# Optimization experiments

Hardware: AMD Instinct MI355X
Metric: run time of the kernel (lower is better)

Reference implementation:

```python
import jax, jax.numpy as jnp
import numpy as np

B = 2048      # number of scenes (samples)
A = 64        # max agents per scene
D = 128       # latent_size (embed dim)
H = 4         # heads (hardcoded in module)
HD = D // H   # head dim = 32
NEG = -1e9


def setup_inputs() -> dict:
    key = jax.random.key(0)
    k1, k2, k3, k4 = jax.random.split(key, 4)
    # flat ragged agent features; only the first sum(agents) rows are 'real'
    att_in = jax.random.normal(k1, (B * A, D), dtype=jnp.float32)
    agents_per_sample = jax.random.randint(k2, (B,), 1, A + 1)  # each scene has >=1 agent
    s = 1.0 / np.sqrt(D)
    w_in = jax.random.uniform(k3, (3 * D, D), minval=-s, maxval=s, dtype=jnp.float32)
    b_in = jnp.zeros((3 * D,), dtype=jnp.float32)
    w_out = jax.random.uniform(k4, (D, D), minval=-s, maxval=s, dtype=jnp.float32)
    b_out = jnp.zeros((D,), dtype=jnp.float32)
    return {"att_in": att_in, "w_in": w_in, "b_in": b_in,
            "w_out": w_out, "b_out": b_out, "agents_per_sample": agents_per_sample}


def reference(att_in, w_in, b_in, w_out, b_out, agents_per_sample):
    # scatter flat ragged rows into padded [B, A, D] (same as padded_att_in[mask] = att_in)
    offsets = jnp.cumsum(agents_per_sample) - agents_per_sample          # exclusive prefix sum
    idx = offsets[:, None] + jnp.arange(A)[None, :]                      # [B, A] flat row index
    mask = jnp.arange(A)[None, :] < agents_per_sample[:, None]          # [B, A] valid-agent mask
    padded = jnp.take(att_in, idx, axis=0) * mask[..., None].astype(att_in.dtype)
    # fused in-projection (nn.MultiheadAttention in_proj)
    qkv = padded @ w_in.T + b_in                                        # [B, A, 3D]
    q, k, v = jnp.split(qkv, 3, axis=-1)
    q = q.reshape(B, A, H, HD)
    k = k.reshape(B, A, H, HD)
    v = v.reshape(B, A, H, HD)
    scores = jnp.einsum('bqhd,bkhd->bhqk', q, k) / np.sqrt(HD).astype(q.dtype)
    # key_padding_mask: padded keys excluded from softmax
    scores = jnp.where(mask[:, None, None, :], scores, NEG)
    attn = jax.nn.softmax(scores, axis=-1)
    ctx = jnp.einsum('bhqk,bkhd->bqhd', attn, v).reshape(B, A, D)
    out = (ctx @ w_out.T + b_out) * mask[..., None].astype(ctx.dtype)   # zero out padded rows (torch slices them off)
    return out
```

## Files before the change

kernel.cpp:

```cpp
#include <hip/hip_runtime.h>
#include <hip/hip_bf16.h>

typedef __bf16 bf16;
typedef __bf16 bf16x4 __attribute__((ext_vector_type(4)));
typedef __bf16 bf16x8 __attribute__((ext_vector_type(8)));
typedef float  f32x4  __attribute__((ext_vector_type(4)));

#define NEG_INF (-1e9f)

#define N_SCENES 2048

__global__ __launch_bounds__(256) void prep_kernel(
    const float* __restrict__ w_in, const float* __restrict__ w_out,
    const int* __restrict__ agents,
    bf16* __restrict__ w_in_b, bf16* __restrict__ w_out_b, int* __restrict__ offs)
{
    __shared__ int tot[256];
    const int t = threadIdx.x;
    if (blockIdx.x == 0) {
        int loc[8]; int s = 0;
        #pragma unroll
        for (int j = 0; j < 8; ++j) { loc[j] = agents[t * 8 + j]; s += loc[j]; }
        tot[t] = s;
        __syncthreads();
        for (int o = 1; o < 256; o <<= 1) {
            int v = (t >= o) ? tot[t - o] : 0;
            __syncthreads();
            tot[t] += v;
            __syncthreads();
        }
        int run = tot[t] - s;
        #pragma unroll
        for (int j = 0; j < 8; ++j) { offs[t * 8 + j] = run; run += loc[j]; }
    } else {
        int i = (blockIdx.x - 1) * 1024 + t * 4;
        float4 v; bf16* dst;
        if (i < 49152) { v = *(const float4*)(w_in + i);            dst = w_in_b + i; }
        else           { v = *(const float4*)(w_out + (i - 49152)); dst = w_out_b + (i - 49152); }
        bf16x4 o = { (bf16)v.x, (bf16)v.y, (bf16)v.z, (bf16)v.w };
        *(bf16x4*)dst = o;
    }
}

__global__ __launch_bounds__(256, 2) void attn_kernel(
    const float* __restrict__ att_in,
    const float* __restrict__ b_in, const float* __restrict__ b_out,
    const bf16* __restrict__ w_in_b, const bf16* __restrict__ w_out_b,
    const int* __restrict__ agents, const int* __restrict__ offs,
    float* __restrict__ out)
{
    __shared__ bf16 s_x[64 * 128];
    __shared__ bf16 s_qk[64 * 256];
    __shared__ bf16 s_vT[128 * 64];
    __shared__ bf16 s_ctx[64 * 128];

    const int b    = blockIdx.x;
    const int tid  = threadIdx.x;
    const int lane = tid & 63;
    const int w    = tid >> 6;
    const int r    = lane & 15;
    const int qd   = lane >> 4;
    const int nb   = agents[b];
    const int off  = offs[b];

    for (int i = tid; i < 64 * 32; i += 256) {
        int row = i >> 5, c4 = i & 31;
        float4 v = make_float4(0.f, 0.f, 0.f, 0.f);
        if (row < nb)
            v = *(const float4*)(att_in + (((size_t)(off + row)) << 7) + (c4 << 2));
        int chunk = c4 >> 1, half = c4 & 1;
        int c = chunk ^ (row & 15);
        bf16x4 o = { (bf16)v.x, (bf16)v.y, (bf16)v.z, (bf16)v.w };
        *(bf16x4*)(s_x + row * 128 + c * 8 + half * 4) = o;
    }
    __syncthreads();

    bf16x8 xa[4][4];
    #pragma unroll
    for (int mt = 0; mt < 4; ++mt)
        #pragma unroll
        for (int ks = 0; ks < 4; ++ks) {
            int row = mt * 16 + r;
            int c = (ks * 4 + qd) ^ r;
            xa[mt][ks] = *(const bf16x8*)(s_x + row * 128 + c * 8);
        }
    #pragma unroll
    for (int t6 = 0; t6 < 6; ++t6) {
        int nt = w + t6 * 4;
        int j0 = nt * 16;
        bf16x8 wb[4];
        #pragma unroll
        for (int ks = 0; ks < 4; ++ks)
            wb[ks] = *(const bf16x8*)(w_in_b + (size_t)(j0 + r) * 128 + ks * 32 + qd * 8);
        float bias = b_in[j0 + r];
        #pragma unroll
        for (int mt = 0; mt < 4; ++mt) {
            f32x4 acc = { 0.f, 0.f, 0.f, 0.f };
            #pragma unroll
            for (int ks = 0; ks < 4; ++ks)
                acc = __builtin_amdgcn_mfma_f32_16x16x32_bf16(xa[mt][ks], wb[ks], acc, 0, 0, 0);
            if (nt < 16) {
                #pragma unroll
                for (int i = 0; i < 4; ++i) {
                    int row = mt * 16 + qd * 4 + i;
                    int c = (nt * 2 + (r >> 3)) ^ (row & 15);
                    s_qk[row * 256 + c * 8 + (r & 7)] = (bf16)(acc[i] + bias);
                }
            } else {
                int hd = j0 + r - 256;
                #pragma unroll
                for (int i = 0; i < 4; ++i) {
                    int agent = mt * 16 + qd * 4 + i;
                    int c = (agent >> 3) ^ (hd & 7);
                    s_vT[hd * 64 + c * 8 + (agent & 7)] = (bf16)(acc[i] + bias);
                }
            }
        }
    }
    __syncthreads();

    const int h = w;
    bf16x8 qa[4], kb[4];
    #pragma unroll
    for (int mt = 0; mt < 4; ++mt) {
        int row = mt * 16 + r;
        int c = (h * 4 + qd) ^ (row & 15);
        qa[mt] = *(const bf16x8*)(s_qk + row * 256 + c * 8);
    }
    #pragma unroll
    for (int nt = 0; nt < 4; ++nt) {
        int row = nt * 16 + r;
        int c = (16 + h * 4 + qd) ^ (row & 15);
        kb[nt] = *(const bf16x8*)(s_qk + row * 256 + c * 8);
    }
    f32x4 S[4][4];
    #pragma unroll
    for (int mt = 0; mt < 4; ++mt)
        #pragma unroll
        for (int nt = 0; nt < 4; ++nt) {
            f32x4 z = { 0.f, 0.f, 0.f, 0.f };
            S[mt][nt] = __builtin_amdgcn_mfma_f32_16x16x32_bf16(qa[mt], kb[nt], z, 0, 0, 0);
        }

    const float scale = 0.17677669529663687f;
    bool kvalid[4];
    #pragma unroll
    for (int nt = 0; nt < 4; ++nt) kvalid[nt] = (nt * 16 + r) < nb;
    #pragma unroll
    for (int mt = 0; mt < 4; ++mt)
        #pragma unroll
        for (int i = 0; i < 4; ++i) {
            float v[4]; float mx = -3e38f;
            #pragma unroll
            for (int nt = 0; nt < 4; ++nt) {
                float val = kvalid[nt] ? S[mt][nt][i] * scale : NEG_INF;
                v[nt] = val; mx = fmaxf(mx, val);
            }
            mx = fmaxf(mx, __shfl_xor(mx, 1));
            mx = fmaxf(mx, __shfl_xor(mx, 2));
            mx = fmaxf(mx, __shfl_xor(mx, 4));
            mx = fmaxf(mx, __shfl_xor(mx, 8));
            float l = 0.f;
            #pragma unroll
            for (int nt = 0; nt < 4; ++nt) { v[nt] = __expf(v[nt] - mx); l += v[nt]; }
            l += __shfl_xor(l, 1); l += __shfl_xor(l, 2);
            l += __shfl_xor(l, 4); l += __shfl_xor(l, 8);
            float rl = 1.0f / l;
            #pragma unroll
            for (int nt = 0; nt < 4; ++nt) S[mt][nt][i] = v[nt] * rl;
        }

    bf16* Pbuf = s_x + w * 2048;
    bf16x8 vb[2][2];
    #pragma unroll
    for (int ks = 0; ks < 2; ++ks)
        #pragma unroll
        for (int n2 = 0; n2 < 2; ++n2) {
            int hdr = h * 32 + n2 * 16 + r;
            int c = (ks * 4 + qd) ^ (hdr & 7);
            vb[ks][n2] = *(const bf16x8*)(s_vT + hdr * 64 + c * 8);
        }
    f32x4 cacc[4][2];
    #pragma unroll
    for (int mt = 0; mt < 4; ++mt)
        #pragma unroll
        for (int n2 = 0; n2 < 2; ++n2)
            cacc[mt][n2] = (f32x4){ 0.f, 0.f, 0.f, 0.f };
    #pragma unroll
    for (int hk = 0; hk < 2; ++hk) {
        #pragma unroll
        for (int mt = 0; mt < 4; ++mt)
            #pragma unroll
            for (int n2 = 0; n2 < 2; ++n2)
                #pragma unroll
                for (int i = 0; i < 4; ++i) {
                    int row = mt * 16 + qd * 4 + i;
                    int col = n2 * 16 + r;
                    int c = (col >> 3) ^ (row & 3);
                    Pbuf[row * 32 + c * 8 + (col & 7)] = (bf16)S[mt][hk * 2 + n2][i];
                }
        bf16x8 pa[4];
        #pragma unroll
        for (int mt = 0; mt < 4; ++mt) {
            int row = mt * 16 + r;
            int c = qd ^ (row & 3);
            pa[mt] = *(const bf16x8*)(Pbuf + row * 32 + c * 8);
        }
        #pragma unroll
        for (int mt = 0; mt < 4; ++mt)
            #pragma unroll
            for (int n2 = 0; n2 < 2; ++n2)
                cacc[mt][n2] = __builtin_amdgcn_mfma_f32_16x16x32_bf16(
                                   pa[mt], vb[hk][n2], cacc[mt][n2], 0, 0, 0);
    }
    #pragma unroll
    for (int mt = 0; mt < 4; ++mt)
        #pragma unroll
        for (int n2 = 0; n2 < 2; ++n2)
            #pragma unroll
            for (int i = 0; i < 4; ++i) {
                int row = mt * 16 + qd * 4 + i;
                int col = h * 32 + n2 * 16 + r;
                int c = (col >> 3) ^ (row & 15);
                s_ctx[row * 128 + c * 8 + (col & 7)] = (bf16)cacc[mt][n2][i];
            }
    __syncthreads();

    bf16x8 ca[4][4];
    #pragma unroll
    for (int mt = 0; mt < 4; ++mt)
        #pragma unroll
        for (int ks = 0; ks < 4; ++ks) {
            int row = mt * 16 + r;
            int c = (ks * 4 + qd) ^ (row & 15);
            ca[mt][ks] = *(const bf16x8*)(s_ctx + row * 128 + c * 8);
        }
    #pragma unroll
    for (int t2 = 0; t2 < 2; ++t2) {
        int nt = w * 2 + t2;
        int j0 = nt * 16;
        bf16x8 wb[4];
        #pragma unroll
        for (int ks = 0; ks < 4; ++ks)
            wb[ks] = *(const bf16x8*)(w_out_b + (size_t)(j0 + r) * 128 + ks * 32 + qd * 8);
        float bias = b_out[j0 + r];
        #pragma unroll
        for (int mt = 0; mt < 4; ++mt) {
            f32x4 acc = { 0.f, 0.f, 0.f, 0.f };
            #pragma unroll
            for (int ks = 0; ks < 4; ++ks)
                acc = __builtin_amdgcn_mfma_f32_16x16x32_bf16(ca[mt][ks], wb[ks], acc, 0, 0, 0);
            #pragma unroll
            for (int i = 0; i < 4; ++i) {
                int row = mt * 16 + qd * 4 + i;
                float val = (row < nb) ? (acc[i] + bias) : 0.f;
                out[((size_t)b * 64 + row) * 128 + j0 + r] = val;
            }
        }
    }
}

extern "C" void kernel_launch(void* const* d_in, const int* in_sizes, int n_in,
                              void* d_out, int out_size, void* d_ws, size_t ws_size,
                              hipStream_t stream)
{
    const float* att_in = (const float*)d_in[0];
    const float* w_in   = (const float*)d_in[1];
    const float* b_in   = (const float*)d_in[2];
    const float* w_out  = (const float*)d_in[3];
    const float* b_out  = (const float*)d_in[4];
    const int*   agents = (const int*)d_in[5];

    bf16* w_in_b  = (bf16*)d_ws;
    bf16* w_out_b = w_in_b + 49152;
    int*  offs    = (int*)((char*)d_ws + 98304 + 32768);

    prep_kernel<<<65, 256, 0, stream>>>(w_in, w_out, agents, w_in_b, w_out_b, offs);
    attn_kernel<<<N_SCENES, 256, 0, stream>>>(att_in, b_in, b_out, w_in_b, w_out_b,
                                              agents, offs, (float*)d_out);
}
```

Measured before the change: 177.7 us.

## Restructure attention per head-wave with ragged tile skipping and smaller LDS

Each wave now computes only its own head's Q, K and V projection columns into a private LDS region, so two block-wide barriers disappear. Input rows are loaded directly from global memory into registers instead of being staged through LDS. All MFMA tiles beyond the scene's real agent count (16-row granularity) are skipped, and padded output rows are written as zeros directly. LDS drops from 80KB to 48KB, which allows raising launch bounds to 3 blocks per CU, at the cost of data-dependent branches and uncoalesced direct global loads.

Measured after the change: 180.4 us. Within noise of the previous version (+1.5%).

```diff
diff --git a/kernel.cpp b/kernel.cpp
--- a/kernel.cpp
+++ b/kernel.cpp
@@ -7,7 +7,6 @@
 typedef float  f32x4  __attribute__((ext_vector_type(4)));
 
 #define NEG_INF (-1e9f)
-
 #define N_SCENES 2048
 
 __global__ __launch_bounds__(256) void prep_kernel(
@@ -42,221 +41,227 @@
     }
 }
 
-__global__ __launch_bounds__(256, 2) void attn_kernel(
+__global__ __launch_bounds__(256, 3) void attn_kernel(
     const float* __restrict__ att_in,
     const float* __restrict__ b_in, const float* __restrict__ b_out,
     const bf16* __restrict__ w_in_b, const bf16* __restrict__ w_out_b,
     const int* __restrict__ agents, const int* __restrict__ offs,
     float* __restrict__ out)
 {
-    __shared__ bf16 s_x[64 * 128];
-    __shared__ bf16 s_qk[64 * 256];
-    __shared__ bf16 s_vT[128 * 64];
-    __shared__ bf16 s_ctx[64 * 128];
+    __shared__ bf16 s_lds[4 * 6144];
 
     const int b    = blockIdx.x;
     const int tid  = threadIdx.x;
     const int lane = tid & 63;
     const int w    = tid >> 6;
+    const int h    = w;
     const int r    = lane & 15;
     const int qd   = lane >> 4;
+    const int r7   = lane & 7;
     const int nb   = agents[b];
     const int off  = offs[b];
-
-    for (int i = tid; i < 64 * 32; i += 256) {
-        int row = i >> 5, c4 = i & 31;
-        float4 v = make_float4(0.f, 0.f, 0.f, 0.f);
-        if (row < nb)
-            v = *(const float4*)(att_in + (((size_t)(off + row)) << 7) + (c4 << 2));
-        int chunk = c4 >> 1, half = c4 & 1;
-        int c = chunk ^ (row & 15);
-        bf16x4 o = { (bf16)v.x, (bf16)v.y, (bf16)v.z, (bf16)v.w };
-        *(bf16x4*)(s_x + row * 128 + c * 8 + half * 4) = o;
-    }
-    __syncthreads();
+    const int mtc  = (nb + 15) >> 4;
+    const int mt16 = mtc << 4;
+
+    bf16* qk = s_lds + w * 6144;
+    bf16* vT = qk + 4096;
+
+    {
+        const float4 z4 = make_float4(0.f, 0.f, 0.f, 0.f);
+        const int nz = (64 - mt16) * 32;
+        for (int i = tid; i < nz; i += 256) {
+            int row = mt16 + (i >> 5);
+            *(float4*)(out + ((size_t)b * 64 + row) * 128 + (i & 31) * 4) = z4;
+        }
+    }
+
+    if (mtc & 1) {
+        int row = lane >> 1, half = lane & 1;
+        int c = (2 * mtc + half) ^ (row & 7);
+        bf16x8 z8 = {(bf16)0.f,(bf16)0.f,(bf16)0.f,(bf16)0.f,
+                     (bf16)0.f,(bf16)0.f,(bf16)0.f,(bf16)0.f};
+        *(bf16x8*)(vT + row * 64 + c * 8) = z8;
+    }
 
     bf16x8 xa[4][4];
     #pragma unroll
     for (int mt = 0; mt < 4; ++mt)
         #pragma unroll
         for (int ks = 0; ks < 4; ++ks) {
+            float4 lo = make_float4(0.f,0.f,0.f,0.f), hi = lo;
             int row = mt * 16 + r;
-            int c = (ks * 4 + qd) ^ r;
-            xa[mt][ks] = *(const bf16x8*)(s_x + row * 128 + c * 8);
-        }
-    #pragma unroll
-    for (int t6 = 0; t6 < 6; ++t6) {
-        int nt = w + t6 * 4;
-        int j0 = nt * 16;
+            if (row < nb) {
+                const float* p = att_in + (((size_t)(off + row)) << 7) + ks * 32 + qd * 8;
+                lo = *(const float4*)p;
+                hi = *(const float4*)(p + 4);
+            }
+            xa[mt][ks] = (bf16x8){(bf16)lo.x,(bf16)lo.y,(bf16)lo.z,(bf16)lo.w,
+                                  (bf16)hi.x,(bf16)hi.y,(bf16)hi.z,(bf16)hi.w};
+        }
+
+    #pragma unroll
+    for (int t = 0; t < 6; ++t) {
+        const int kind = t >> 1, sub = t & 1;
+        const int j0 = kind * 128 + h * 32 + sub * 16;
         bf16x8 wb[4];
         #pragma unroll
         for (int ks = 0; ks < 4; ++ks)
             wb[ks] = *(const bf16x8*)(w_in_b + (size_t)(j0 + r) * 128 + ks * 32 + qd * 8);
-        float bias = b_in[j0 + r];
+        const float bias = b_in[j0 + r];
         #pragma unroll
         for (int mt = 0; mt < 4; ++mt) {
-            f32x4 acc = { 0.f, 0.f, 0.f, 0.f };
-            #pragma unroll
-            for (int ks = 0; ks < 4; ++ks)
-                acc = __builtin_amdgcn_mfma_f32_16x16x32_bf16(xa[mt][ks], wb[ks], acc, 0, 0, 0);
-            if (nt < 16) {
+            if (mt < mtc) {
+                f32x4 acc = {0.f, 0.f, 0.f, 0.f};
+                #pragma unroll
+                for (int ks = 0; ks < 4; ++ks)
+                    acc = __builtin_amdgcn_mfma_f32_16x16x32_bf16(xa[mt][ks], wb[ks], acc, 0, 0, 0);
+                if (kind < 2) {
+                    int chunk = kind * 4 + sub * 2 + (r >> 3);
+                    #pragma unroll
+                    for (int i = 0; i < 4; ++i) {
+                        int row = mt * 16 + qd * 4 + i;
+                        int c = chunk ^ (row & 7);
+                        qk[row * 64 + c * 8 + r7] = (bf16)(acc[i] + bias);
+                    }
+                } else {
+                    int row = sub * 16 + r;
+                    int c = (2 * mt + (qd >> 1)) ^ r7;
+                    bf16x4 pk = {(bf16)(acc[0]+bias), (bf16)(acc[1]+bias),
+                                 (bf16)(acc[2]+bias), (bf16)(acc[3]+bias)};
+                    *(bf16x4*)(vT + row * 64 + c * 8 + (qd & 1) * 4) = pk;
+                }
+            }
+        }
+    }
+
+    bf16x8 qa[4], kb[4];
+    #pragma unroll
+    for (int mt = 0; mt < 4; ++mt)
+        if (mt < mtc) {
+            int row = mt * 16 + r;
+            qa[mt] = *(const bf16x8*)(qk + row * 64 + ((qd) ^ r7) * 8);
+            kb[mt] = *(const bf16x8*)(qk + row * 64 + ((4 + qd) ^ r7) * 8);
+        }
+    f32x4 S[4][4];
+    #pragma unroll
+    for (int mt = 0; mt < 4; ++mt)
+        if (mt < mtc)
+            #pragma unroll
+            for (int nt = 0; nt < 4; ++nt)
+                if (nt < mtc) {
+                    f32x4 z = {0.f, 0.f, 0.f, 0.f};
+                    S[mt][nt] = __builtin_amdgcn_mfma_f32_16x16x32_bf16(qa[mt], kb[nt], z, 0, 0, 0);
+                }
+
+    const float scale = 0.17677669529663687f;
+    bool kvalid[4];
+    #pragma unroll
+    for (int nt = 0; nt < 4; ++nt) kvalid[nt] = (nt < mtc) && ((nt * 16 + r) < nb);
+    #pragma unroll
+    for (int mt = 0; mt < 4; ++mt)
+        if (mt < mtc)
+            #pragma unroll
+            for (int i = 0; i < 4; ++i) {
+                float v[4]; float mx = NEG_INF;
+                #pragma unroll
+                for (int nt = 0; nt < 4; ++nt) {
+                    float val = kvalid[nt] ? S[mt][nt][i] * scale : NEG_INF;
+                    v[nt] = val; mx = fmaxf(mx, val);
+                }
+                mx = fmaxf(mx, __shfl_xor(mx, 1));
+                mx = fmaxf(mx, __shfl_xor(mx, 2));
+                mx = fmaxf(mx, __shfl_xor(mx, 4));
+                mx = fmaxf(mx, __shfl_xor(mx, 8));
+                float l = 0.f;
+                #pragma unroll
+                for (int nt = 0; nt < 4; ++nt) { v[nt] = __expf(v[nt] - mx); l += v[nt]; }
+                l += __shfl_xor(l, 1); l += __shfl_xor(l, 2);
+                l += __shfl_xor(l, 4); l += __shfl_xor(l, 8);
+                float rl = 1.0f / l;
+                #pragma unroll
+                for (int nt = 0; nt < 4; ++nt) S[mt][nt][i] = v[nt] * rl;
+            }
+
+    f32x4 cacc[4][2];
+    #pragma unroll
+    for (int mt = 0; mt < 4; ++mt)
+        #pragma unroll
+        for (int n2 = 0; n2 < 2; ++n2)
+            cacc[mt][n2] = (f32x4){0.f, 0.f, 0.f, 0.f};
+    const int hkc = (mtc + 1) >> 1;
+    #pragma unroll
+    for (int hk = 0; hk < 2; ++hk)
+        if (hk < hkc) {
+            #pragma unroll
+            for (int mt = 0; mt < 4; ++mt)
+                if (mt < mtc)
+                    #pragma unroll
+                    for (int n2 = 0; n2 < 2; ++n2) {
+                        int chunk = 4 + n2 * 2 + (r >> 3);
+                        #pragma unroll
+                        for (int i = 0; i < 4; ++i) {
+                            int row = mt * 16 + qd * 4 + i;
+                            int c = chunk ^ (row & 7);
+                            qk[row * 64 + c * 8 + r7] = (bf16)S[mt][hk * 2 + n2][i];
+                        }
+                    }
+            bf16x8 vb[2];
+            #pragma unroll
+            for (int n2 = 0; n2 < 2; ++n2) {
+                int row = n2 * 16 + r;
+                int c = (hk * 4 + qd) ^ r7;
+                vb[n2] = *(const bf16x8*)(vT + row * 64 + c * 8);
+            }
+            #pragma unroll
+            for (int mt = 0; mt < 4; ++mt)
+                if (mt < mtc) {
+                    int row = mt * 16 + r;
+                    bf16x8 pa = *(const bf16x8*)(qk + row * 64 + ((4 + qd) ^ r7) * 8);
+                    cacc[mt][0] = __builtin_amdgcn_mfma_f32_16x16x32_bf16(pa, vb[0], cacc[mt][0], 0, 0, 0);
+                    cacc[mt][1] = __builtin_amdgcn_mfma_f32_16x16x32_bf16(pa, vb[1], cacc[mt][1], 0, 0, 0);
+                }
+        }
+
+    #pragma unroll
+    for (int mt = 0; mt < 4; ++mt)
+        if (mt < mtc)
+            #pragma unroll
+            for (int n2 = 0; n2 < 2; ++n2) {
+                int chunk = n2 * 2 + (r >> 3);
                 #pragma unroll
                 for (int i = 0; i < 4; ++i) {
                     int row = mt * 16 + qd * 4 + i;
-                    int c = (nt * 2 + (r >> 3)) ^ (row & 15);
-                    s_qk[row * 256 + c * 8 + (r & 7)] = (bf16)(acc[i] + bias);
-                }
-            } else {
-                int hd = j0 + r - 256;
-                #pragma unroll
-                for (int i = 0; i < 4; ++i) {
-                    int agent = mt * 16 + qd * 4 + i;
-                    int c = (agent >> 3) ^ (hd & 7);
-                    s_vT[hd * 64 + c * 8 + (agent & 7)] = (bf16)(acc[i] + bias);
-                }
-            }
-        }
-    }
+                    int c = chunk ^ (row & 7);
+                    qk[row * 64 + c * 8 + r7] = (bf16)cacc[mt][n2][i];
+                }
+            }
     __syncthreads();
 
-    const int h = w;
-    bf16x8 qa[4], kb[4];
-    #pragma unroll
-    for (int mt = 0; mt < 4; ++mt) {
-        int row = mt * 16 + r;
-        int c = (h * 4 + qd) ^ (row & 15);
-        qa[mt] = *(const bf16x8*)(s_qk + row * 256 + c * 8);
-    }
-    #pragma unroll
-    for (int nt = 0; nt < 4; ++nt) {
-        int row = nt * 16 + r;
-        int c = (16 + h * 4 + qd) ^ (row & 15);
-        kb[nt] = *(const bf16x8*)(s_qk + row * 256 + c * 8);
-    }
-    f32x4 S[4][4];
-    #pragma unroll
-    for (int mt = 0; mt < 4; ++mt)
-        #pragma unroll
-        for (int nt = 0; nt < 4; ++nt) {
-            f32x4 z = { 0.f, 0.f, 0.f, 0.f };
-            S[mt][nt] = __builtin_amdgcn_mfma_f32_16x16x32_bf16(qa[mt], kb[nt], z, 0, 0, 0);
-        }
-
-    const float scale = 0.17677669529663687f;
-    bool kvalid[4];
-    #pragma unroll
-    for (int nt = 0; nt < 4; ++nt) kvalid[nt] = (nt * 16 + r) < nb;
-    #pragma unroll
-    for (int mt = 0; mt < 4; ++mt)
-        #pragma unroll
-        for (int i = 0; i < 4; ++i) {
-            float v[4]; float mx = -3e38f;
-            #pragma unroll
-            for (int nt = 0; nt < 4; ++nt) {
-                float val = kvalid[nt] ? S[mt][nt][i] * scale : NEG_INF;
-                v[nt] = val; mx = fmaxf(mx, val);
-            }
-            mx = fmaxf(mx, __shfl_xor(mx, 1));
-            mx = fmaxf(mx, __shfl_xor(mx, 2));
-            mx = fmaxf(mx, __shfl_xor(mx, 4));
-            mx = fmaxf(mx, __shfl_xor(mx, 8));
-            float l = 0.f;
-            #pragma unroll
-            for (int nt = 0; nt < 4; ++nt) { v[nt] = __expf(v[nt] - mx); l += v[nt]; }
-            l += __shfl_xor(l, 1); l += __shfl_xor(l, 2);
-            l += __shfl_xor(l, 4); l += __shfl_xor(l, 8);
-            float rl = 1.0f / l;
-            #pragma unroll
-            for (int nt = 0; nt < 4; ++nt) S[mt][nt][i] = v[nt] * rl;
-        }
-
-    bf16* Pbuf = s_x + w * 2048;
-    bf16x8 vb[2][2];
-    #pragma unroll
-    for (int ks = 0; ks < 2; ++ks)
-        #pragma unroll
-        for (int n2 = 0; n2 < 2; ++n2) {
-            int hdr = h * 32 + n2 * 16 + r;
-            int c = (ks * 4 + qd) ^ (hdr & 7);
-            vb[ks][n2] = *(const bf16x8*)(s_vT + hdr * 64 + c * 8);
-        }
-    f32x4 cacc[4][2];
-    #pragma unroll
-    for (int mt = 0; mt < 4; ++mt)
-        #pragma unroll
-        for (int n2 = 0; n2 < 2; ++n2)
-            cacc[mt][n2] = (f32x4){ 0.f, 0.f, 0.f, 0.f };
-    #pragma unroll
-    for (int hk = 0; hk < 2; ++hk) {
+    #pragma unroll
+    for (int t2 = 0; t2 < 2; ++t2) {
+        const int j0 = (w * 2 + t2) * 16;
+        bf16x8 wo[4];
+        #pragma unroll
+        for (int ks = 0; ks < 4; ++ks)
+            wo[ks] = *(const bf16x8*)(w_out_b + (size_t)(j0 + r) * 128 + ks * 32 + qd * 8);
+        const float bias = b_out[j0 + r];
         #pragma unroll
         for (int mt = 0; mt < 4; ++mt)
-            #pragma unroll
-            for (int n2 = 0; n2 < 2; ++n2)
+            if (mt < mtc) {
+                f32x4 acc = {0.f, 0.f, 0.f, 0.f};
+                #pragma unroll
+                for (int ks = 0; ks < 4; ++ks) {
+                    int row = mt * 16 + r;
+                    bf16x8 ca = *(const bf16x8*)(s_lds + ks * 6144 + row * 64 + (qd ^ r7) * 8);
+                    acc = __builtin_amdgcn_mfma_f32_16x16x32_bf16(ca, wo[ks], acc, 0, 0, 0);
+                }
                 #pragma unroll
                 for (int i = 0; i < 4; ++i) {
                     int row = mt * 16 + qd * 4 + i;
-                    int col = n2 * 16 + r;
-                    int c = (col >> 3) ^ (row & 3);
-                    Pbuf[row * 32 + c * 8 + (col & 7)] = (bf16)S[mt][hk * 2 + n2][i];
-                }
-        bf16x8 pa[4];
-        #pragma unroll
-        for (int mt = 0; mt < 4; ++mt) {
-            int row = mt * 16 + r;
-            int c = qd ^ (row & 3);
-            pa[mt] = *(const bf16x8*)(Pbuf + row * 32 + c * 8);
-        }
-        #pragma unroll
-        for (int mt = 0; mt < 4; ++mt)
-            #pragma unroll
-            for (int n2 = 0; n2 < 2; ++n2)
-                cacc[mt][n2] = __builtin_amdgcn_mfma_f32_16x16x32_bf16(
-                                   pa[mt], vb[hk][n2], cacc[mt][n2], 0, 0, 0);
-    }
-    #pragma unroll
-    for (int mt = 0; mt < 4; ++mt)
-        #pragma unroll
-        for (int n2 = 0; n2 < 2; ++n2)
-            #pragma unroll
-            for (int i = 0; i < 4; ++i) {
-                int row = mt * 16 + qd * 4 + i;
-                int col = h * 32 + n2 * 16 + r;
-                int c = (col >> 3) ^ (row & 15);
-                s_ctx[row * 128 + c * 8 + (col & 7)] = (bf16)cacc[mt][n2][i];
-            }
-    __syncthreads();
-
-    bf16x8 ca[4][4];
-    #pragma unroll
-    for (int mt = 0; mt < 4; ++mt)
-        #pragma unroll
-        for (int ks = 0; ks < 4; ++ks) {
-            int row = mt * 16 + r;
-            int c = (ks * 4 + qd) ^ (row & 15);
-            ca[mt][ks] = *(const bf16x8*)(s_ctx + row * 128 + c * 8);
-        }
-    #pragma unroll
-    for (int t2 = 0; t2 < 2; ++t2) {
-        int nt = w * 2 + t2;
-        int j0 = nt * 16;
-        bf16x8 wb[4];
-        #pragma unroll
-        for (int ks = 0; ks < 4; ++ks)
-            wb[ks] = *(const bf16x8*)(w_out_b + (size_t)(j0 + r) * 128 + ks * 32 + qd * 8);
-        float bias = b_out[j0 + r];
-        #pragma unroll
-        for (int mt = 0; mt < 4; ++mt) {
-            f32x4 acc = { 0.f, 0.f, 0.f, 0.f };
-            #pragma unroll
-            for (int ks = 0; ks < 4; ++ks)
-                acc = __builtin_amdgcn_mfma_f32_16x16x32_bf16(ca[mt][ks], wb[ks], acc, 0, 0, 0);
-            #pragma unroll
-            for (int i = 0; i < 4; ++i) {
-                int row = mt * 16 + qd * 4 + i;
-                float val = (row < nb) ? (acc[i] + bias) : 0.f;
-                out[((size_t)b * 64 + row) * 128 + j0 + r] = val;
-            }
-        }
+                    float val = (row < nb) ? (acc[i] + bias) : 0.f;
+                    out[((size_t)b * 64 + row) * 128 + j0 + r] = val;
+                }
+            }
     }
 }
 
```
